# Performance work log

Hardware: AMD Instinct MI355X
Metric: run time of the kernel (lower is better)

## Reference

```python
import jax, jax.numpy as jnp
import numpy as np

HIDDEN = 3072
N_HEADS = 24
N_KV = 8
HEAD_DIM = HIDDEN // N_HEADS          # 128
ROT = int(HEAD_DIM * 0.75)            # 96 (partial rotary)
OP_SIZE = N_HEADS * HEAD_DIM + 2 * N_KV * HEAD_DIM  # 5120
LORA_R = 256
LORA_SCALE = 512.0 / LORA_R           # 2.0
ROPE_THETA = 10000.0
SCALE = HEAD_DIM ** -0.5


def setup_inputs() -> dict:
    key = jax.random.key(0)
    ks = jax.random.split(key, 8)
    B, S = 2, 2048
    hidden_states = jax.random.normal(ks[0], (B, S, HIDDEN), dtype=jnp.float32)
    position_ids = jnp.arange(B * S, dtype=jnp.int64 if jax.config.jax_enable_x64 else jnp.int32).reshape(B, S)
    w = lambda k, o, i: jax.random.normal(k, (o, i), dtype=jnp.float32) * (i ** -0.5)
    return {
        "hidden_states": hidden_states,
        "Wqkv": w(ks[1], OP_SIZE, HIDDEN),
        "Aqkv": w(ks[2], LORA_R, HIDDEN),
        "Bqkv": w(ks[3], OP_SIZE, LORA_R) * 0.01,
        "Wo": w(ks[4], HIDDEN, N_HEADS * HEAD_DIM),
        "Ao": w(ks[5], LORA_R, N_HEADS * HEAD_DIM),
        "Bo": w(ks[6], HIDDEN, LORA_R) * 0.01,
        "position_ids": position_ids,
    }


def _lora_linear(x, W, A, Bm):
    # base GEMM + low-rank LoRA update, scaling = alpha/r
    return x @ W.T + (x @ A.T) @ Bm.T * LORA_SCALE


def _rotate_half(x):
    h = x.shape[-1] // 2
    return jnp.concatenate((-x[..., h:], x[..., :h]), axis=-1)


def reference(hidden_states, Wqkv, Aqkv, Bqkv, Wo, Ao, Bo, position_ids):
    B, S, _ = hidden_states.shape
    qkv = _lora_linear(hidden_states, Wqkv, Aqkv, Bqkv)  # [B,S,5120]
    q_pos = N_HEADS * HEAD_DIM
    kv_pos = N_KV * HEAD_DIM
    q = qkv[..., :q_pos].reshape(B, S, N_HEADS, HEAD_DIM)
    k = qkv[..., q_pos:q_pos + kv_pos].reshape(B, S, N_KV, HEAD_DIM)
    v = qkv[..., q_pos + kv_pos:].reshape(B, S, N_KV, HEAD_DIM)

    # partial RoPE: cos/sin cache over rotary_ndims=96
    inv_freq = 1.0 / (ROPE_THETA ** (jnp.arange(0, ROT, 2, dtype=jnp.float32) / ROT))  # [48]
    freqs = position_ids.astype(jnp.float32)[..., None] * inv_freq  # [B,S,48]
    emb = jnp.concatenate((freqs, freqs), axis=-1)                   # [B,S,96]
    cos = jnp.cos(emb)[:, :, None, :]  # broadcast over head axis (bsnd)
    sin = jnp.sin(emb)[:, :, None, :]

    def rope(x):
        xr, xp = x[..., :ROT], x[..., ROT:]
        xr = xr * cos + _rotate_half(xr) * sin
        return jnp.concatenate((xr, xp), axis=-1)

    q = rope(q)
    k = rope(k)

    # GQA: repeat kv heads to match query heads
    groups = N_HEADS // N_KV
    k = jnp.repeat(k, groups, axis=2)
    v = jnp.repeat(v, groups, axis=2)

    scores = jnp.einsum('bqhd,bkhd->bhqk', q, k) * SCALE  # [B,H,S,S]
    causal = jnp.tril(jnp.ones((S, S), dtype=bool))
    scores = jnp.where(causal, scores, jnp.finfo(scores.dtype).min)
    probs = jax.nn.softmax(scores, axis=-1)
    attn = jnp.einsum('bhqk,bkhd->bqhd', probs, v).reshape(B, S, N_HEADS * HEAD_DIM)
    return _lora_linear(attn, Wo, Ao, Bo)
```

## Files before the change

kernel.cpp:

```cpp
#include <hip/hip_runtime.h>

typedef unsigned short u16;
typedef unsigned int   u32;

typedef __bf16 bf16_t;
typedef bf16_t bf16x8 __attribute__((ext_vector_type(8)));
typedef float  f32x4  __attribute__((ext_vector_type(4)));
typedef float  f32x16 __attribute__((ext_vector_type(16)));
typedef u16    u16x8  __attribute__((ext_vector_type(8)));
typedef u32    u32x4  __attribute__((ext_vector_type(4)));

__device__ __forceinline__ float bf2f(u16 u) { return __uint_as_float(((u32)u) << 16); }
__device__ __forceinline__ u16 f2bf(float f) {
  u32 u = __float_as_uint(f);
  u32 r = u + 0x7fffu + ((u >> 16) & 1u);
  return (u16)(r >> 16);
}
__device__ __forceinline__ float fast_exp2(float x) { return __builtin_amdgcn_exp2f(x); }

__device__ __forceinline__ void gload_lds16(const u16* g, u16* l) {
  __builtin_amdgcn_global_load_lds(
      (const __attribute__((address_space(1))) void*)g,
      (__attribute__((address_space(3))) void*)l,
      16, 0, 0);
}

#define SBAR0() __builtin_amdgcn_sched_barrier(0)
#define HWBAR() __builtin_amdgcn_s_barrier()

__global__ void k_cast_all(const float* __restrict__ x,  const float* __restrict__ wq,
                           const float* __restrict__ bq, const float* __restrict__ aq,
                           const float* __restrict__ wo, const float* __restrict__ bo,
                           const float* __restrict__ ao,
                           u16* __restrict__ xw, u16* __restrict__ wwq, u16* __restrict__ aqkvb,
                           u16* __restrict__ wwo, u16* __restrict__ aob) {
  const int total = 5177344;
  int i = blockIdx.x * blockDim.x + threadIdx.x;
  const int stride = gridDim.x * blockDim.x;
  for (; i < total; i += stride) {
    const float* src; u16* dst; int r, c8, L, off, sL;
    if (i < 1572864)      { int loc = i;           r = loc / 384; c8 = loc - r * 384; src = x;  dst = xw;    L = 3328; off = 0;    sL = 3072; }
    else if (i < 3538944) { int loc = i - 1572864; r = loc / 384; c8 = loc - r * 384; src = wq; dst = wwq;   L = 3328; off = 0;    sL = 3072; }
    else if (i < 3702784) { int loc = i - 3538944; r = loc >> 5;  c8 = loc & 31;      src = bq; dst = wwq;   L = 3328; off = 3072; sL = 256;  }
    else if (i < 3801088) { int loc = i - 3702784; r = loc / 384; c8 = loc - r * 384; src = aq; dst = aqkvb; L = 3072; off = 0;    sL = 3072; }
    else if (i < 4980736) { int loc = i - 3801088; r = loc / 384; c8 = loc - r * 384; src = wo; dst = wwo;   L = 3328; off = 0;    sL = 3072; }
    else if (i < 5079040) { int loc = i - 4980736; r = loc >> 5;  c8 = loc & 31;      src = bo; dst = wwo;   L = 3328; off = 3072; sL = 256;  }
    else                  { int loc = i - 5079040; r = loc / 384; c8 = loc - r * 384; src = ao; dst = aob;   L = 3072; off = 0;    sL = 3072; }
    const f32x4* p = (const f32x4*)(src + (size_t)r * sL + c8 * 8);
    f32x4 a = p[0], b2 = p[1];
    u16x8 o;
    o[0] = f2bf(a[0]);  o[1] = f2bf(a[1]);  o[2] = f2bf(a[2]);  o[3] = f2bf(a[3]);
    o[4] = f2bf(b2[0]); o[5] = f2bf(b2[1]); o[6] = f2bf(b2[2]); o[7] = f2bf(b2[3]);
    *(u16x8*)(dst + (size_t)r * L + off + c8 * 8) = o;
  }
}

__global__ void k_red4_cast(const float* __restrict__ t4, u16* __restrict__ out,
                            int C8, int L, int off, float scale, size_t plane) {
  const int r  = blockIdx.y;
  const int c8 = blockIdx.x * 64 + threadIdx.x;
  if (c8 >= C8) return;
  size_t base = (size_t)r * (C8 * 8) + c8 * 8;
  float s[8];
#pragma unroll
  for (int j = 0; j < 8; ++j) s[j] = 0.f;
#pragma unroll
  for (int p = 0; p < 4; ++p) {
    const f32x4* q = (const f32x4*)(t4 + p * plane + base);
    f32x4 a = q[0], b = q[1];
    s[0] += a[0]; s[1] += a[1]; s[2] += a[2]; s[3] += a[3];
    s[4] += b[0]; s[5] += b[1]; s[6] += b[2]; s[7] += b[3];
  }
  u16x8 o;
#pragma unroll
  for (int j = 0; j < 8; ++j) o[j] = f2bf(s[j] * scale);
  *(u16x8*)(out + (size_t)r * L + off + c8 * 8) = o;
}

__global__ __launch_bounds__(256) void k_gemm_bt_sk(
    const u16* __restrict__ A, const u16* __restrict__ B, float* __restrict__ C,
    int M, int N, int lda, int ldb, int kc) {
  __shared__ u16 As[64][64 + 8];
  __shared__ u16 Bs[64][64 + 8];
  const int tid   = threadIdx.x;
  const int lane  = tid & 63;
  const int w     = tid >> 6;
  const int wm    = (w >> 1) * 32;
  const int wn    = (w & 1) * 32;
  const int row16 = lane & 15;
  const int quad  = lane >> 4;
  const int m0 = blockIdx.y * 64;
  const int n0 = blockIdx.x * 64;
  const int ldr = tid >> 2;
  const int ldc = (tid & 3) * 16;
  const int z   = blockIdx.z;
  float* Cz = C + (size_t)z * M * N;
  const int kbeg = z * kc, kend = kbeg + kc;

  f32x4 acc[2][2] = {};

  for (int k0 = kbeg; k0 < kend; k0 += 64) {
    const u16* ga = A + (size_t)(m0 + ldr) * lda + (k0 + ldc);
    const u16* gb = B + (size_t)(n0 + ldr) * ldb + (k0 + ldc);
    u16x8 a0 = *(const u16x8*)ga;
    u16x8 a1 = *(const u16x8*)(ga + 8);
    u16x8 b0 = *(const u16x8*)gb;
    u16x8 b1 = *(const u16x8*)(gb + 8);
    __syncthreads();
    *(u16x8*)&As[ldr][ldc]     = a0;
    *(u16x8*)&As[ldr][ldc + 8] = a1;
    *(u16x8*)&Bs[ldr][ldc]     = b0;
    *(u16x8*)&Bs[ldr][ldc + 8] = b1;
    __syncthreads();
#pragma unroll
    for (int kk = 0; kk < 64; kk += 32) {
      bf16x8 af0 = *(const bf16x8*)&As[wm + row16][kk + quad * 8];
      bf16x8 af1 = *(const bf16x8*)&As[wm + 16 + row16][kk + quad * 8];
      bf16x8 bg0 = *(const bf16x8*)&Bs[wn + row16][kk + quad * 8];
      bf16x8 bg1 = *(const bf16x8*)&Bs[wn + 16 + row16][kk + quad * 8];
      acc[0][0] = __builtin_amdgcn_mfma_f32_16x16x32_bf16(af0, bg0, acc[0][0], 0, 0, 0);
      acc[0][1] = __builtin_amdgcn_mfma_f32_16x16x32_bf16(af0, bg1, acc[0][1], 0, 0, 0);
      acc[1][0] = __builtin_amdgcn_mfma_f32_16x16x32_bf16(af1, bg0, acc[1][0], 0, 0, 0);
      acc[1][1] = __builtin_amdgcn_mfma_f32_16x16x32_bf16(af1, bg1, acc[1][1], 0, 0, 0);
    }
  }
#pragma unroll
  for (int tm = 0; tm < 2; ++tm)
#pragma unroll
    for (int tn = 0; tn < 2; ++tn) {
      int gm = m0 + wm + tm * 16 + quad * 4;
      int gn = n0 + wn + tn * 16 + row16;
#pragma unroll
      for (int r = 0; r < 4; ++r)
        Cz[(size_t)(gm + r) * N + gn] = acc[tm][tn][r];
    }
}

__device__ __forceinline__ void stage_half(
    int H, int nt4,
    const u16* __restrict__ A, const u16* __restrict__ B, int S,
    int m0, int n0, u16* AsB, u16* BsB,
    int w, int rowin, int colsw) {
  if (H >= nt4) return;
  const int t = H >> 2, slot = H & 3;
  const int half = slot & 1;
  const u16* G = (slot < 2) ? A : B;
  const int r0 = (slot < 2) ? m0 : n0;
  u16* lds = ((slot < 2) ? AsB : BsB) + (t & 1) * 16384 + half * 8192;
  const int k0 = t * 64;
#pragma unroll
  for (int i = 0; i < 2; ++i) {
    const int chunk = w * 2 + i;
    const int row = half * 128 + chunk * 8 + rowin;
    gload_lds16(G + (size_t)(r0 + row) * S + k0 + colsw, lds + chunk * 512);
  }
}

__device__ __forceinline__ bf16x8 frag_ld(const u16* base, int row, int c16) {
  return *(const bf16x8*)(base + row * 64 + ((c16 ^ (row & 7)) << 3));
}

template <int RB>
__device__ __forceinline__ void gemm256_group(
    int k, int nt,
    const u16* __restrict__ A, const u16* __restrict__ B, int S,
    int m0, int n0, u16* AsB, u16* BsB,
    int wr, int wc, int row16, int quad, int w, int rowin, int colsw,
    f32x4 (&acc)[8][4]) {
  const u16* Ab = AsB + RB * 16384;
  const u16* Bb = BsB + RB * 16384;
  const int nt4 = nt * 4;
  bf16x8 a0[4][2], a1[4][2], b0[2][2], b1[2][2];

#pragma unroll
  for (int mf = 0; mf < 4; ++mf)
#pragma unroll
    for (int kk = 0; kk < 2; ++kk)
      a0[mf][kk] = frag_ld(Ab, wr * 128 + mf * 16 + row16, kk * 4 + quad);
#pragma unroll
  for (int nf = 0; nf < 2; ++nf)
#pragma unroll
    for (int kk = 0; kk < 2; ++kk)
      b0[nf][kk] = frag_ld(Bb, wc * 64 + nf * 16 + row16, kk * 4 + quad);
  stage_half(4 * k + 5, nt4, A, B, S, m0, n0, AsB, BsB, w, rowin, colsw);
  SBAR0(); HWBAR(); SBAR0();
  __builtin_amdgcn_s_setprio(1);
#pragma unroll
  for (int mf = 0; mf < 4; ++mf)
#pragma unroll
    for (int nf = 0; nf < 2; ++nf)
#pragma unroll
      for (int kk = 0; kk < 2; ++kk)
        acc[mf][nf] = __builtin_amdgcn_mfma_f32_16x16x32_bf16(a0[mf][kk], b0[nf][kk], acc[mf][nf], 0, 0, 0);
  __builtin_amdgcn_s_setprio(0);
  SBAR0(); HWBAR(); SBAR0();

#pragma unroll
  for (int nf = 0; nf < 2; ++nf)
#pragma unroll
    for (int kk = 0; kk < 2; ++kk)
      b1[nf][kk] = frag_ld(Bb, wc * 64 + 32 + nf * 16 + row16, kk * 4 + quad);
  stage_half(4 * k + 6, nt4, A, B, S, m0, n0, AsB, BsB, w, rowin, colsw);
  SBAR0(); HWBAR(); SBAR0();
  __builtin_amdgcn_s_setprio(1);
#pragma unroll
  for (int mf = 0; mf < 4; ++mf)
#pragma unroll
    for (int nf = 0; nf < 2; ++nf)
#pragma unroll
      for (int kk = 0; kk < 2; ++kk)
        acc[mf][2 + nf] = __builtin_amdgcn_mfma_f32_16x16x32_bf16(a0[mf][kk], b1[nf][kk], acc[mf][2 + nf], 0, 0, 0);
  __builtin_amdgcn_s_setprio(0);
  SBAR0(); HWBAR(); SBAR0();

#pragma unroll
  for (int mf = 0; mf < 4; ++mf)
#pragma unroll
    for (int kk = 0; kk < 2; ++kk)
      a1[mf][kk] = frag_ld(Ab, wr * 128 + 64 + mf * 16 + row16, kk * 4 + quad);
  stage_half(4 * k + 7, nt4, A, B, S, m0, n0, AsB, BsB, w, rowin, colsw);
  SBAR0(); HWBAR(); SBAR0();
  __builtin_amdgcn_s_setprio(1);
#pragma unroll
  for (int mf = 0; mf < 4; ++mf)
#pragma unroll
    for (int nf = 0; nf < 2; ++nf)
#pragma unroll
      for (int kk = 0; kk < 2; ++kk)
        acc[4 + mf][nf] = __builtin_amdgcn_mfma_f32_16x16x32_bf16(a1[mf][kk], b0[nf][kk], acc[4 + mf][nf], 0, 0, 0);
  __builtin_amdgcn_s_setprio(0);
  SBAR0(); HWBAR(); SBAR0();

  stage_half(4 * k + 8, nt4, A, B, S, m0, n0, AsB, BsB, w, rowin, colsw);
  SBAR0();
  if (k < nt - 2) { asm volatile("s_waitcnt vmcnt(2)" ::: "memory"); }
  else            { asm volatile("s_waitcnt vmcnt(0)" ::: "memory"); }
  HWBAR(); SBAR0();
  __builtin_amdgcn_s_setprio(1);
#pragma unroll
  for (int mf = 0; mf < 4; ++mf)
#pragma unroll
    for (int nf = 0; nf < 2; ++nf)
#pragma unroll
      for (int kk = 0; kk < 2; ++kk)
        acc[4 + mf][2 + nf] = __builtin_amdgcn_mfma_f32_16x16x32_bf16(a1[mf][kk], b1[nf][kk], acc[4 + mf][2 + nf], 0, 0, 0);
  __builtin_amdgcn_s_setprio(0);
  SBAR0(); HWBAR(); SBAR0();
}

template <int BF16OUT>
__device__ __forceinline__ void gemm256_run(
    const u16* __restrict__ A, const u16* __restrict__ B, int S, int nt,
    int m0, int n0, void* __restrict__ Cp, int ldc, int cn0,
    u16* As, u16* Bs) {
  const int tid   = threadIdx.x;
  const int lane  = tid & 63;
  const int w     = tid >> 6;
  const int wr    = w >> 2;
  const int wc    = w & 3;
  const int row16 = lane & 15;
  const int quad  = lane >> 4;
  const int rowin = lane >> 3;
  const int colsw = ((lane & 7) ^ (lane >> 3)) << 3;

  f32x4 acc[8][4] = {};

#pragma unroll
  for (int H = 0; H < 5; ++H)
    stage_half(H, nt * 4, A, B, S, m0, n0, As, Bs, w, rowin, colsw);
  asm volatile("s_waitcnt vmcnt(2)" ::: "memory");
  HWBAR(); SBAR0();

  int k = 0;
  for (; k + 1 < nt; k += 2) {
    gemm256_group<0>(k,     nt, A, B, S, m0, n0, As, Bs, wr, wc, row16, quad, w, rowin, colsw, acc);
    gemm256_group<1>(k + 1, nt, A, B, S, m0, n0, As, Bs, wr, wc, row16, quad, w, rowin, colsw, acc);
  }
  if (k < nt)
    gemm256_group<0>(k, nt, A, B, S, m0, n0, As, Bs, wr, wc, row16, quad, w, rowin, colsw, acc);

#pragma unroll
  for (int mi = 0; mi < 8; ++mi) {
    const int gm = m0 + wr * 128 + mi * 16 + quad * 4;
#pragma unroll
    for (int nj = 0; nj < 4; ++nj) {
      const int gn = cn0 + wc * 64 + nj * 16 + row16;
#pragma unroll
      for (int r = 0; r < 4; ++r) {
        if (BF16OUT) ((u16*)Cp)[(size_t)(gm + r) * ldc + gn] = f2bf(acc[mi][nj][r]);
        else         ((float*)Cp)[(size_t)(gm + r) * ldc + gn] = acc[mi][nj][r];
      }
    }
  }
}

__global__ __launch_bounds__(512, 2) void k_gemm256(
    const u16* __restrict__ A, const u16* __restrict__ B, float* __restrict__ C,
    int M, int N, int K) {
  __shared__ u16 As[2 * 16384];
  __shared__ u16 Bs[2 * 16384];
  const int nwg = (int)gridDim.x;
  const int bid = (int)blockIdx.x;
  const int xcd = bid & 7, rest = bid >> 3;
  const int qq = nwg >> 3, rr = nwg & 7;
  const int wg = (xcd < rr ? xcd * (qq + 1) : rr * (qq + 1) + (xcd - rr) * qq) + rest;
  const int nbx = N >> 8;
  const int m0 = (wg / nbx) << 8;
  const int n0 = (wg % nbx) << 8;
  gemm256_run<0>(A, B, K, K >> 6, m0, n0, C, N, n0, As, Bs);
}

__global__ __launch_bounds__(512, 2) void k_gemm256_qkv(
    const u16* __restrict__ A, const u16* __restrict__ B,
    float* __restrict__ Cqk, u16* __restrict__ Cvp) {
  __shared__ u16 As[2 * 16384];
  __shared__ u16 Bs[2 * 16384];
  const int bid = (int)blockIdx.x;
  const int xcd = bid & 7, rest = bid >> 3;
  const int wg = xcd * 32 + rest;
  const int m0 = (wg >> 4) << 8;
  const int n0 = (wg & 15) << 8;
  gemm256_run<0>(A, B, 3328, 52, m0, n0, Cqk, 4096, n0, As, Bs);
  if (bid >= 128) return;
  __syncthreads();
  const int m  = bid & 15;
  const int nv = (bid >> 4) & 3;
  const int kc = bid >> 6;
  const u16* At = A + kc * 1664;
  const u16* Bt = B + (size_t)4096 * 3328 + kc * 1664;
  gemm256_run<1>(At, Bt, 3328, 26, m * 256, nv * 256,
                 Cvp + (size_t)kc * 4096 * 1024, 1024, nv * 256, As, Bs);
}

__global__ void k_rope_tab(const int* __restrict__ pos_ids, float* __restrict__ tab,
                           int* __restrict__ ctr) {
  if (blockIdx.x == 0 && threadIdx.x == 0) *ctr = 0;
  const int t = threadIdx.x;
  const int r = blockIdx.x * 4 + t / 48;
  const int j = t % 48;
  const float pos = (float)pos_ids[r];
  float invf = powf(10000.0f, -(float)j * (1.0f / 48.0f));
  float e = pos * invf;
  tab[(size_t)r * 96 + j]      = cosf(e);
  tab[(size_t)r * 96 + 48 + j] = sinf(e);
}

__global__ void k_rope_v(const float* __restrict__ qk, const u16* __restrict__ vp,
                         const float* __restrict__ tab,
                         u16* __restrict__ qb, u16* __restrict__ kb, u16* __restrict__ vtg) {
  const int y = blockIdx.y;
  const int d = threadIdx.x;
  if (y < 32) {
    const int r  = blockIdx.x;
    const int hh = y;
    const float* src;
    if (hh < 24) src = qk + (size_t)r * 4096 + hh * 128;
    else         src = qk + (size_t)r * 4096 + 3072 + (hh - 24) * 128;
    float x = src[d];
    float outv;
    if (d >= 96) {
      outv = x;
    } else {
      int j = (d < 48) ? d : d - 48;
      float c  = tab[(size_t)r * 96 + j];
      float sn = tab[(size_t)r * 96 + 48 + j];
      if (d < 48) outv = x * c - src[d + 48] * sn;
      else        outv = x * c + src[d - 48] * sn;
    }
    u16 o = f2bf(outv);
    if (hh < 24) qb[((size_t)r * 24 + hh) * 128 + d] = o;
    else         kb[((size_t)r * 8 + (hh - 24)) * 128 + d] = o;
  } else {
    const int bk = blockIdx.x >> 8;
    const int kg = blockIdx.x & 255;
    const int b = bk >> 3, kvh = bk & 7;
    const u16* s0 = vp + (size_t)(b * 2048 + kg * 8) * 1024 + kvh * 128 + d;
    const u16* s1 = s0 + (size_t)4096 * 1024;
    u16x8 pack;
#pragma unroll
    for (int t = 0; t < 8; ++t)
      pack[t] = f2bf(bf2f(s0[(size_t)t * 1024]) + bf2f(s1[(size_t)t * 1024]));
    *(u16x8*)(vtg + ((size_t)bk * 128 + d) * 2048 + kg * 8) = pack;
  }
}

#define NJOBS 768

__global__ __launch_bounds__(256) void k_attn_mfma(
    const u16* __restrict__ qb, const u16* __restrict__ kb, const u16* __restrict__ vtg,
    u16* __restrict__ attnw, int* __restrict__ ctr) {
  __shared__ u16 Ks0[8192], Ks1[8192];
  __shared__ u16 Vt0[8192], Vt1[8192];
  __shared__ int s_job;

  const int tid  = threadIdx.x;
  const int lane = tid & 63;
  const int w    = tid >> 6;
  const int l31  = lane & 31;
  const int hi   = lane >> 5;
  const int r7   = lane & 7;
  const float C1 = 0.08838834764831845f * 1.4426950408889634f;

  for (;;) {
    if (tid == 0) s_job = atomicAdd(ctr, 1);
    __syncthreads();
    const int j = s_job;
    if (j >= NJOBS) return;

    const int qt  = 15 - (j / 48);
    const int bh  = j % 48;
    const int b   = bh / 24;
    const int h   = bh % 24;
    const int kvh = h / 3;
    const int q0  = qt * 128;
    const int qrow = q0 + w * 32 + l31;

    const u16* qrb = qb + (((size_t)(b * 2048 + qrow)) * 24 + h) * 128;
    bf16x8 qf[8];
#pragma unroll
    for (int kk = 0; kk < 8; ++kk) qf[kk] = *(const bf16x8*)(qrb + kk * 16 + hi * 8);

    const u16* kbbase = kb + ((size_t)(b * 2048) * 8 + kvh) * 128;
    const u16* vtbase = vtg + (size_t)(b * 8 + kvh) * 128 * 2048;

    f32x16 o32[4] = {};
    float m_st = -INFINITY, l_st = 0.f;
    const int ntile = 2 * qt + 2;

#define STAGE_K(Kd, KB0)                                                        \
  { _Pragma("unroll") for (int i = 0; i < 4; ++i) {                             \
      const int c = w * 4 + i;                                                  \
      const int rowk = 4 * c + (lane >> 4);                                     \
      gload_lds16(kbbase + (size_t)((KB0) + rowk) * 1024 +                      \
                      (((lane & 15) ^ (rowk & 7)) << 3),                        \
                  (Kd) + c * 512); } }
#define STAGE_V(Vd, KB0)                                                        \
  { _Pragma("unroll") for (int i = 0; i < 4; ++i) {                             \
      const int c = w * 4 + i;                                                  \
      const int rowv = 8 * c + (lane >> 3);                                     \
      gload_lds16(vtbase + (size_t)rowv * 2048 + (KB0) +                        \
                      (((lane & 7) ^ (rowv & 7)) << 3),                         \
                  (Vd) + c * 512); } }

    STAGE_K(Ks0, 0);
    STAGE_V(Vt0, 0);

    for (int t = 0; t < ntile; ++t) {
      const int kb0 = t * 64;
      const u16* Kc = (t & 1) ? Ks1 : Ks0;
      const u16* Vc = (t & 1) ? Vt1 : Vt0;

      asm volatile("s_waitcnt vmcnt(0)" ::: "memory");
      SBAR0(); HWBAR(); SBAR0();
      if (t + 1 < ntile) {
        u16* Kn = (t & 1) ? Ks0 : Ks1;
        u16* Vn = (t & 1) ? Vt0 : Vt1;
        STAGE_K(Kn, kb0 + 64);
        STAGE_V(Vn, kb0 + 64);
      }
      SBAR0();

      f32x16 s0 = {}, s1 = {};
      __builtin_amdgcn_s_setprio(1);
#pragma unroll
      for (int kk = 0; kk < 8; ++kk) {
        bf16x8 kf0 = *(const bf16x8*)&Kc[l31 * 128 + (((2 * kk + hi) ^ r7) << 3)];
        s0 = __builtin_amdgcn_mfma_f32_32x32x16_bf16(kf0, qf[kk], s0, 0, 0, 0);
        bf16x8 kf1 = *(const bf16x8*)&Kc[(32 + l31) * 128 + (((2 * kk + hi) ^ ((32 + l31) & 7)) << 3)];
        s1 = __builtin_amdgcn_mfma_f32_32x32x16_bf16(kf1, qf[kk], s1, 0, 0, 0);
      }
      __builtin_amdgcn_s_setprio(0);

      if (kb0 >= q0) {
#pragma unroll
        for (int r = 0; r < 16; ++r) {
          const int crow = (r & 3) + 8 * (r >> 2) + 4 * hi;
          if (kb0 + crow > qrow)      s0[r] = -INFINITY;
          if (kb0 + 32 + crow > qrow) s1[r] = -INFINITY;
        }
      }

      float tm[8];
#pragma unroll
      for (int r = 0; r < 8; ++r)
        tm[r] = fmaxf(fmaxf(s0[r], s0[r + 8]), fmaxf(s1[r], s1[r + 8]));
#pragma unroll
      for (int st = 4; st >= 1; st >>= 1)
#pragma unroll
        for (int r = 0; r < 4; ++r)
          if (r < st) tm[r] = fmaxf(tm[r], tm[r + st]);
      float mx = fmaxf(tm[0], __shfl_xor(tm[0], 32));

      const bool skip = __all((mx - m_st) * C1 <= 8.0f);
      if (!skip) {
        const float mnew = fmaxf(m_st, mx);
        const float alpha = fast_exp2((m_st - mnew) * C1);
        l_st *= alpha;
#pragma unroll
        for (int dt = 0; dt < 4; ++dt)
#pragma unroll
          for (int r = 0; r < 16; ++r) o32[dt][r] *= alpha;
        m_st = mnew;
      }
      const float mc = m_st * C1;
      float ts[8];
#pragma unroll
      for (int r = 0; r < 16; ++r) {
        s0[r] = fast_exp2(__builtin_fmaf(s0[r], C1, -mc));
        s1[r] = fast_exp2(__builtin_fmaf(s1[r], C1, -mc));
      }
#pragma unroll
      for (int r = 0; r < 8; ++r) ts[r] = (s0[r] + s0[r + 8]) + (s1[r] + s1[r + 8]);
#pragma unroll
      for (int st = 4; st >= 1; st >>= 1)
#pragma unroll
        for (int r = 0; r < 4; ++r)
          if (r < st) ts[r] += ts[r + st];
      l_st += ts[0] + __shfl_xor(ts[0], 32);

#pragma unroll
      for (int kt = 0; kt < 2; ++kt) {
        const f32x16& sv = kt ? s1 : s0;
        u32 pk[8];
#pragma unroll
        for (int i = 0; i < 8; ++i)
          asm("v_cvt_pk_bf16_f32 %0, %1, %2"
              : "=v"(pk[i]) : "v"(sv[2 * i]), "v"(sv[2 * i + 1]));
        u32 e0 = __shfl_xor(hi ? pk[0] : pk[2], 32);
        u32 e1 = __shfl_xor(hi ? pk[1] : pk[3], 32);
        u32 e2 = __shfl_xor(hi ? pk[4] : pk[6], 32);
        u32 e3 = __shfl_xor(hi ? pk[5] : pk[7], 32);
        u32x4 w0, w1;
        w0[0] = hi ? e0 : pk[0]; w0[1] = hi ? e1 : pk[1];
        w0[2] = hi ? pk[2] : e0; w0[3] = hi ? pk[3] : e1;
        w1[0] = hi ? e2 : pk[4]; w1[1] = hi ? e3 : pk[5];
        w1[2] = hi ? pk[6] : e2; w1[3] = hi ? pk[7] : e3;
        bf16x8 pb0 = __builtin_bit_cast(bf16x8, w0);
        bf16x8 pb1 = __builtin_bit_cast(bf16x8, w1);
        __builtin_amdgcn_s_setprio(1);
#pragma unroll
        for (int dt = 0; dt < 4; ++dt) {
          const int vrow = dt * 32 + l31;
          bf16x8 vf0 = *(const bf16x8*)&Vc[vrow * 64 + (((2 * (2 * kt) + hi) ^ (vrow & 7)) << 3)];
          o32[dt] = __builtin_amdgcn_mfma_f32_32x32x16_bf16(vf0, pb0, o32[dt], 0, 0, 0);
          bf16x8 vf1 = *(const bf16x8*)&Vc[vrow * 64 + (((2 * (2 * kt + 1) + hi) ^ (vrow & 7)) << 3)];
          o32[dt] = __builtin_amdgcn_mfma_f32_32x32x16_bf16(vf1, pb1, o32[dt], 0, 0, 0);
        }
        __builtin_amdgcn_s_setprio(0);
      }
    }

    __syncthreads();
    const float inv = 1.0f / l_st;
    u16* scr = ((w < 2) ? Ks0 : Ks1) + (w & 1) * 4096;
#pragma unroll
    for (int dt = 0; dt < 4; ++dt)
#pragma unroll
      for (int r = 0; r < 16; ++r) {
        const int d = 32 * dt + (r & 3) + 8 * (r >> 2) + 4 * hi;
        const int slot = (d >> 3) ^ (l31 & 7);
        scr[l31 * 128 + slot * 8 + (d & 7)] = f2bf(o32[dt][r] * inv);
      }
    const int q32r = lane >> 1, part = lane & 1;
    const size_t grow = ((size_t)(b * 2048 + q0 + w * 32 + q32r)) * 3328 + (size_t)h * 128;
#pragma unroll
    for (int c = 0; c < 8; ++c) {
      const int d0 = part * 64 + c * 8;
      const int s2 = (d0 >> 3) ^ (q32r & 7);
      *(u16x8*)(attnw + grow + d0) = *(const u16x8*)&scr[q32r * 128 + s2 * 8];
    }
  }
}

#define OFF_XW    ((size_t)0)
#define OFF_WWQ   ((size_t)27262976)
#define OFF_AQKVB ((size_t)61341696)
#define OFF_WWO   ((size_t)62914560)
#define OFF_AOB   ((size_t)83361792)
#define OFF_QKV   ((size_t)84934656)
#define OFF_CVP   (OFF_QKV + (size_t)67108864)
#define OFF_TA4   OFF_QKV
#define OFF_QB    OFF_XW
#define OFF_KB    OFF_WWQ
#define OFF_VTG   (OFF_WWQ + (size_t)8388608)
#define OFF_RTAB  (OFF_WWQ + (size_t)16777216)
#define OFF_CTR   (OFF_WWQ + (size_t)18350080)
#define OFF_ATTNW OFF_QKV
#define OFF_TO4   (OFF_QKV + (size_t)27262976)

extern "C" void kernel_launch(void* const* d_in, const int* in_sizes, int n_in,
                              void* d_out, int out_size, void* d_ws, size_t ws_size,
                              hipStream_t stream) {
  const float* x    = (const float*)d_in[0];
  const float* Wqkv = (const float*)d_in[1];
  const float* Aqkv = (const float*)d_in[2];
  const float* Bqkv = (const float*)d_in[3];
  const float* Wo   = (const float*)d_in[4];
  const float* Ao   = (const float*)d_in[5];
  const float* Bo   = (const float*)d_in[6];
  const int*   pos  = (const int*)d_in[7];
  float* out = (float*)d_out;
  char* ws = (char*)d_ws;

  u16* xw    = (u16*)(ws + OFF_XW);
  u16* wwq   = (u16*)(ws + OFF_WWQ);
  u16* aqkvb = (u16*)(ws + OFF_AQKVB);
  u16* wwo   = (u16*)(ws + OFF_WWO);
  u16* aob   = (u16*)(ws + OFF_AOB);
  float* qk  = (float*)(ws + OFF_QKV);
  u16* cvp   = (u16*)(ws + OFF_CVP);
  float* tA4 = (float*)(ws + OFF_TA4);
  u16* qb    = (u16*)(ws + OFF_QB);
  u16* kb    = (u16*)(ws + OFF_KB);
  u16* vtg   = (u16*)(ws + OFF_VTG);
  float* rtab = (float*)(ws + OFF_RTAB);
  int* ctr   = (int*)(ws + OFF_CTR);
  u16* attnw = (u16*)(ws + OFF_ATTNW);
  float* tO4 = (float*)(ws + OFF_TO4);

  k_cast_all<<<2048, 256, 0, stream>>>(x, Wqkv, Bqkv, Aqkv, Wo, Bo, Ao,
                                       xw, wwq, aqkvb, wwo, aob);

  k_gemm_bt_sk<<<dim3(4, 64, 4), 256, 0, stream>>>(xw, aqkvb, tA4, 4096, 256, 3328, 3072, 768);
  k_red4_cast<<<dim3(1, 4096), 64, 0, stream>>>(tA4, xw, 32, 3328, 3072, 2.f, (size_t)4096 * 256);

  k_gemm256_qkv<<<dim3(256), 512, 0, stream>>>(xw, wwq, qk, cvp);

  k_rope_tab<<<dim3(1024), 192, 0, stream>>>(pos, rtab, ctr);
  k_rope_v<<<dim3(4096, 33), 128, 0, stream>>>(qk, cvp, rtab, qb, kb, vtg);

  k_attn_mfma<<<dim3(512), 256, 0, stream>>>(qb, kb, vtg, attnw, ctr);

  k_gemm_bt_sk<<<dim3(4, 64, 4), 256, 0, stream>>>(attnw, aob, tO4, 4096, 256, 3328, 3072, 768);
  k_red4_cast<<<dim3(1, 4096), 64, 0, stream>>>(tO4, attnw, 32, 3328, 3072, 2.f, (size_t)4096 * 256);

  k_gemm256<<<dim3((3072 / 256) * (4096 / 256)), 512, 0, stream>>>(attnw, wwo, out, 4096, 3072, 3328);
}
```

Measured before the change: 652.0 us.

## Deepen GEMM prefetch and overlap V split-K GEMM with RoPE in one kernel

The GEMM main loop now issues two half-tile stages in pairs at later slots, keeping more global loads in flight (vmcnt 8 instead of 2, eight prologue stages). The V-projection split-K GEMM that used to run serially after the QK GEMM in the same kernel moves to a new kernel whose other blocks apply RoPE to Q and K concurrently. The V transpose becomes its own kernel, and Q/K bf16 buffers are placed in the output buffer as scratch. This adds a launch and relies on the changed stage ordering keeping the LDS double-buffer hazards correct.

```diff
diff --git a/kernel.cpp b/kernel.cpp
--- a/kernel.cpp
+++ b/kernel.cpp
@@ -182,7 +182,6 @@
 #pragma unroll
     for (int kk = 0; kk < 2; ++kk)
       b0[nf][kk] = frag_ld(Bb, wc * 64 + nf * 16 + row16, kk * 4 + quad);
-  stage_half(4 * k + 5, nt4, A, B, S, m0, n0, AsB, BsB, w, rowin, colsw);
   SBAR0(); HWBAR(); SBAR0();
   __builtin_amdgcn_s_setprio(1);
 #pragma unroll
@@ -200,7 +199,6 @@
 #pragma unroll
     for (int kk = 0; kk < 2; ++kk)
       b1[nf][kk] = frag_ld(Bb, wc * 64 + 32 + nf * 16 + row16, kk * 4 + quad);
-  stage_half(4 * k + 6, nt4, A, B, S, m0, n0, AsB, BsB, w, rowin, colsw);
   SBAR0(); HWBAR(); SBAR0();
   __builtin_amdgcn_s_setprio(1);
 #pragma unroll
@@ -218,7 +216,8 @@
 #pragma unroll
     for (int kk = 0; kk < 2; ++kk)
       a1[mf][kk] = frag_ld(Ab, wr * 128 + 64 + mf * 16 + row16, kk * 4 + quad);
-  stage_half(4 * k + 7, nt4, A, B, S, m0, n0, AsB, BsB, w, rowin, colsw);
+  stage_half(4 * k + 10, nt4, A, B, S, m0, n0, AsB, BsB, w, rowin, colsw);
+  stage_half(4 * k + 11, nt4, A, B, S, m0, n0, AsB, BsB, w, rowin, colsw);
   SBAR0(); HWBAR(); SBAR0();
   __builtin_amdgcn_s_setprio(1);
 #pragma unroll
@@ -232,8 +231,9 @@
   SBAR0(); HWBAR(); SBAR0();
 
   stage_half(4 * k + 8, nt4, A, B, S, m0, n0, AsB, BsB, w, rowin, colsw);
+  stage_half(4 * k + 9, nt4, A, B, S, m0, n0, AsB, BsB, w, rowin, colsw);
   SBAR0();
-  if (k < nt - 2) { asm volatile("s_waitcnt vmcnt(2)" ::: "memory"); }
+  if (k < nt - 2) { asm volatile("s_waitcnt vmcnt(8)" ::: "memory"); }
   else            { asm volatile("s_waitcnt vmcnt(0)" ::: "memory"); }
   HWBAR(); SBAR0();
   __builtin_amdgcn_s_setprio(1);
@@ -266,9 +266,9 @@
   f32x4 acc[8][4] = {};
 
 #pragma unroll
-  for (int H = 0; H < 5; ++H)
+  for (int H = 0; H < 8; ++H)
     stage_half(H, nt * 4, A, B, S, m0, n0, As, Bs, w, rowin, colsw);
-  asm volatile("s_waitcnt vmcnt(2)" ::: "memory");
+  asm volatile("s_waitcnt vmcnt(8)" ::: "memory");
   HWBAR(); SBAR0();
 
   int k = 0;
@@ -311,8 +311,7 @@
 }
 
 __global__ __launch_bounds__(512, 2) void k_gemm256_qkv(
-    const u16* __restrict__ A, const u16* __restrict__ B,
-    float* __restrict__ Cqk, u16* __restrict__ Cvp) {
+    const u16* __restrict__ A, const u16* __restrict__ B, float* __restrict__ Cqk) {
   __shared__ u16 As[2 * 16384];
   __shared__ u16 Bs[2 * 16384];
   const int bid = (int)blockIdx.x;
@@ -321,15 +320,49 @@
   const int m0 = (wg >> 4) << 8;
   const int n0 = (wg & 15) << 8;
   gemm256_run<0>(A, B, 3328, 52, m0, n0, Cqk, 4096, n0, As, Bs);
-  if (bid >= 128) return;
-  __syncthreads();
-  const int m  = bid & 15;
-  const int nv = (bid >> 4) & 3;
-  const int kc = bid >> 6;
-  const u16* At = A + kc * 1664;
-  const u16* Bt = B + (size_t)4096 * 3328 + kc * 1664;
-  gemm256_run<1>(At, Bt, 3328, 26, m * 256, nv * 256,
-                 Cvp + (size_t)kc * 4096 * 1024, 1024, nv * 256, As, Bs);
+}
+
+__global__ __launch_bounds__(512, 2) void k_qkv2(
+    const u16* __restrict__ A, const u16* __restrict__ B,
+    const float* __restrict__ qkf, u16* __restrict__ Cvp,
+    const float* __restrict__ tab, u16* __restrict__ qb, u16* __restrict__ kb) {
+  __shared__ u16 As[2 * 16384];
+  __shared__ u16 Bs[2 * 16384];
+  const int bid = (int)blockIdx.x;
+  if (bid < 128) {
+    const int m  = bid & 15;
+    const int nv = (bid >> 4) & 3;
+    const int kc = bid >> 6;
+    const u16* At = A + kc * 1664;
+    const u16* Bt = B + (size_t)4096 * 3328 + kc * 1664;
+    gemm256_run<1>(At, Bt, 3328, 26, m * 256, nv * 256,
+                   Cvp + (size_t)kc * 4096 * 1024, 1024, nv * 256, As, Bs);
+  } else {
+    const int rb = bid - 128;
+    const int g  = threadIdx.x >> 7;
+    const int d  = threadIdx.x & 127;
+    for (int u = rb * 4 + g; u < 131072; u += 512) {
+      const int r  = u >> 5;
+      const int hh = u & 31;
+      const float* src;
+      if (hh < 24) src = qkf + (size_t)r * 4096 + hh * 128;
+      else         src = qkf + (size_t)r * 4096 + 3072 + (hh - 24) * 128;
+      float x = src[d];
+      float outv;
+      if (d >= 96) {
+        outv = x;
+      } else {
+        int j = (d < 48) ? d : d - 48;
+        float c  = tab[(size_t)r * 96 + j];
+        float sn = tab[(size_t)r * 96 + 48 + j];
+        if (d < 48) outv = x * c - src[d + 48] * sn;
+        else        outv = x * c + src[d - 48] * sn;
+      }
+      u16 o = f2bf(outv);
+      if (hh < 24) qb[((size_t)r * 24 + hh) * 128 + d] = o;
+      else         kb[((size_t)r * 8 + (hh - 24)) * 128 + d] = o;
+    }
+  }
 }
 
 __global__ void k_rope_tab(const int* __restrict__ pos_ids, float* __restrict__ tab,
@@ -345,43 +378,18 @@
   tab[(size_t)r * 96 + 48 + j] = sinf(e);
 }
 
-__global__ void k_rope_v(const float* __restrict__ qk, const u16* __restrict__ vp,
-                         const float* __restrict__ tab,
-                         u16* __restrict__ qb, u16* __restrict__ kb, u16* __restrict__ vtg) {
-  const int y = blockIdx.y;
-  const int d = threadIdx.x;
-  if (y < 32) {
-    const int r  = blockIdx.x;
-    const int hh = y;
-    const float* src;
-    if (hh < 24) src = qk + (size_t)r * 4096 + hh * 128;
-    else         src = qk + (size_t)r * 4096 + 3072 + (hh - 24) * 128;
-    float x = src[d];
-    float outv;
-    if (d >= 96) {
-      outv = x;
-    } else {
-      int j = (d < 48) ? d : d - 48;
-      float c  = tab[(size_t)r * 96 + j];
-      float sn = tab[(size_t)r * 96 + 48 + j];
-      if (d < 48) outv = x * c - src[d + 48] * sn;
-      else        outv = x * c + src[d - 48] * sn;
-    }
-    u16 o = f2bf(outv);
-    if (hh < 24) qb[((size_t)r * 24 + hh) * 128 + d] = o;
-    else         kb[((size_t)r * 8 + (hh - 24)) * 128 + d] = o;
-  } else {
-    const int bk = blockIdx.x >> 8;
-    const int kg = blockIdx.x & 255;
-    const int b = bk >> 3, kvh = bk & 7;
-    const u16* s0 = vp + (size_t)(b * 2048 + kg * 8) * 1024 + kvh * 128 + d;
-    const u16* s1 = s0 + (size_t)4096 * 1024;
-    u16x8 pack;
-#pragma unroll
-    for (int t = 0; t < 8; ++t)
-      pack[t] = f2bf(bf2f(s0[(size_t)t * 1024]) + bf2f(s1[(size_t)t * 1024]));
-    *(u16x8*)(vtg + ((size_t)bk * 128 + d) * 2048 + kg * 8) = pack;
-  }
+__global__ void k_vtrans(const u16* __restrict__ vp, u16* __restrict__ vtg) {
+  const int d  = threadIdx.x;
+  const int kg = blockIdx.x;
+  const int bk = blockIdx.y;
+  const int b = bk >> 3, kvh = bk & 7;
+  const u16* s0 = vp + (size_t)(b * 2048 + kg * 8) * 1024 + kvh * 128 + d;
+  const u16* s1 = s0 + (size_t)4096 * 1024;
+  u16x8 pack;
+#pragma unroll
+  for (int t = 0; t < 8; ++t)
+    pack[t] = f2bf(bf2f(s0[(size_t)t * 1024]) + bf2f(s1[(size_t)t * 1024]));
+  *(u16x8*)(vtg + ((size_t)bk * 128 + d) * 2048 + kg * 8) = pack;
 }
 
 #define NJOBS 768
@@ -579,12 +587,10 @@
 #define OFF_AOB   ((size_t)83361792)
 #define OFF_QKV   ((size_t)84934656)
 #define OFF_CVP   (OFF_QKV + (size_t)67108864)
+#define OFF_RTAB  (OFF_CVP + (size_t)16777216)
+#define OFF_CTR   (OFF_RTAB + (size_t)1572864)
 #define OFF_TA4   OFF_QKV
-#define OFF_QB    OFF_XW
-#define OFF_KB    OFF_WWQ
 #define OFF_VTG   (OFF_WWQ + (size_t)8388608)
-#define OFF_RTAB  (OFF_WWQ + (size_t)16777216)
-#define OFF_CTR   (OFF_WWQ + (size_t)18350080)
 #define OFF_ATTNW OFF_QKV
 #define OFF_TO4   (OFF_QKV + (size_t)27262976)
 
@@ -609,14 +615,14 @@
   u16* aob   = (u16*)(ws + OFF_AOB);
   float* qk  = (float*)(ws + OFF_QKV);
   u16* cvp   = (u16*)(ws + OFF_CVP);
-  float* tA4 = (float*)(ws + OFF_TA4);
-  u16* qb    = (u16*)(ws + OFF_QB);
-  u16* kb    = (u16*)(ws + OFF_KB);
-  u16* vtg   = (u16*)(ws + OFF_VTG);
   float* rtab = (float*)(ws + OFF_RTAB);
   int* ctr   = (int*)(ws + OFF_CTR);
+  float* tA4 = (float*)(ws + OFF_TA4);
+  u16* vtg   = (u16*)(ws + OFF_VTG);
   u16* attnw = (u16*)(ws + OFF_ATTNW);
   float* tO4 = (float*)(ws + OFF_TO4);
+  u16* qb    = (u16*)d_out;
+  u16* kb    = (u16*)((char*)d_out + 25165824);
 
   k_cast_all<<<2048, 256, 0, stream>>>(x, Wqkv, Bqkv, Aqkv, Wo, Bo, Ao,
                                        xw, wwq, aqkvb, wwo, aob);
@@ -624,10 +630,13 @@
   k_gemm_bt_sk<<<dim3(4, 64, 4), 256, 0, stream>>>(xw, aqkvb, tA4, 4096, 256, 3328, 3072, 768);
   k_red4_cast<<<dim3(1, 4096), 64, 0, stream>>>(tA4, xw, 32, 3328, 3072, 2.f, (size_t)4096 * 256);
 
-  k_gemm256_qkv<<<dim3(256), 512, 0, stream>>>(xw, wwq, qk, cvp);
-
   k_rope_tab<<<dim3(1024), 192, 0, stream>>>(pos, rtab, ctr);
-  k_rope_v<<<dim3(4096, 33), 128, 0, stream>>>(qk, cvp, rtab, qb, kb, vtg);
+
+  k_gemm256_qkv<<<dim3(256), 512, 0, stream>>>(xw, wwq, qk);
+
+  k_qkv2<<<dim3(256), 512, 0, stream>>>(xw, wwq, qk, cvp, rtab, qb, kb);
+
+  k_vtrans<<<dim3(256, 16), 128, 0, stream>>>(cvp, vtg);
 
   k_attn_mfma<<<dim3(512), 256, 0, stream>>>(qb, kb, vtg, attnw, ctr);
 
```

Measured after the change: 734.0 us. +12.6%, slower.
